# Kernel tuning notes

Measured on AMD Instinct MI355X. Metric: run time of the kernel, lower is better.

Reference implementation:

```python
import jax, jax.numpy as jnp
from jax import lax
import numpy as np


def gen_position(p, pos_decay=1.0):
    # Fixed relative-position bias: (9, p*p), neighbor order di*3+dj
    ar = jnp.arange(p, dtype=jnp.float32)
    right = jnp.broadcast_to(jnp.exp(-ar / (p / pos_decay))[None, :], (p, p))  # decays along width
    down = right.T                                                             # decays along height
    i, j = jnp.meshgrid(ar, ar, indexing='ij')
    br = jnp.exp(-(i + j) / (p / pos_decay))
    ones = jnp.ones((p, p), jnp.float32)
    merge = jnp.stack([
        jnp.rot90(br, 2), down[::-1, :], jnp.rot90(br, 1),
        right[:, ::-1], ones, right,
        jnp.rot90(br, 3), down, br,
    ], axis=0)
    return merge.reshape(9, -1)


def attention_conv(x, w_qkv, b_qkv, head_w, window_size, num_heads):
    b, c, h, w = x.shape
    p = window_size // 3
    pad_h = (p * (1 + h // p) - h) % p
    pad_w = (p * (1 + w // p) - w) % p
    xp = jnp.pad(x, ((0, 0), (0, 0), (p + pad_h, p), (p + pad_w, p)), mode='reflect')
    Hp, Wp = xp.shape[2], xp.shape[3]
    nH, nW = Hp // p - 2, Wp // p - 2  # == number of unfold windows (stride p, size 3p)
    # Non-overlapping p x p tiles; each window = 3x3 grid of adjacent tiles.
    tiles = xp.reshape(b, c, nH + 2, p, nW + 2, p).transpose(0, 2, 4, 1, 3, 5)  # [b,nH+2,nW+2,c,p,p]
    neigh = jnp.stack([tiles[:, di:di + nH, dj:dj + nW]
                       for di in range(3) for dj in range(3)], axis=3)  # [b,nH,nW,9,c,p,p]
    L = c * p * p
    pp = p * p
    xw = neigh.reshape(b * nH * nW, 9, L)
    qkv = xw @ w_qkv.T + b_qkv                                  # [N,9,nh*3*L]
    qkv = qkv.reshape(-1, 9, num_heads, 3, c, pp).transpose(0, 2, 4, 3, 1, 5)  # [N,nh,C,3,9,pp]
    q, k, v = qkv[:, :, :, 0], qkv[:, :, :, 1], qkv[:, :, :, 2]  # each [N,nh,C,9,pp]
    bias = gen_position(p)                                       # [9,pp]
    core_q = q[:, :, :, 4, :]                                    # center patch query [N,nh,C,pp]
    score = jnp.einsum('nhcp,nhckp->nhck', core_q, k * bias) / jnp.sqrt(jnp.float32(L))
    attn = jax.nn.softmax(score, axis=-1)                        # over 9 neighbors
    out = jnp.einsum('nhck,nhckp->nhcp', attn, v).reshape(-1, num_heads, L)
    out = jnp.einsum('h,nhd->nd', head_w[0], out)                # head mixing [N,L]
    out = out.reshape(b, nH, nW, c, p, p).transpose(0, 3, 1, 4, 2, 5).reshape(b, c, nH * p, nW * p)
    return out[:, :, pad_h:, pad_w:]


def setup_inputs() -> dict:
    key = jax.random.key(0)
    ks = jax.random.split(key, 8)
    B, C, H, W = 4, 3, 256, 256
    x = jax.random.uniform(ks[0], (B, C, H, W), dtype=jnp.float32)
    # conv3: window 3, p=1, heads 6, L=3 ; conv6: window 6, p=2, heads 4, L=12 ; conv9: window 9, p=3, heads 2, L=27
    w3_qkv = jax.random.normal(ks[1], (6 * 3 * 3, 3), jnp.float32) * 0.2
    b3_qkv = jnp.zeros((6 * 3 * 3,), jnp.float32)
    hw3 = jnp.full((1, 6), 1.0 / 6.0, jnp.float32)
    w6_qkv = jax.random.normal(ks[2], (4 * 3 * 12, 12), jnp.float32) * 0.1
    b6_qkv = jnp.zeros((4 * 3 * 12,), jnp.float32)
    hw6 = jnp.full((1, 4), 1.0 / 4.0, jnp.float32)
    w9_qkv = jax.random.normal(ks[3], (2 * 3 * 27, 27), jnp.float32) * 0.07
    b9_qkv = jnp.zeros((2 * 3 * 27,), jnp.float32)
    hw9 = jnp.full((1, 2), 1.0 / 2.0, jnp.float32)
    conv0_w = jax.random.normal(ks[4], (3, 9, 5, 5), jnp.float32) * 0.05
    conv0_b = jnp.zeros((3,), jnp.float32)
    return {"x": x, "w3_qkv": w3_qkv, "b3_qkv": b3_qkv, "hw3": hw3,
            "w6_qkv": w6_qkv, "b6_qkv": b6_qkv, "hw6": hw6,
            "w9_qkv": w9_qkv, "b9_qkv": b9_qkv, "hw9": hw9,
            "conv0_w": conv0_w, "conv0_b": conv0_b}


def reference(x, w3_qkv, b3_qkv, hw3, w6_qkv, b6_qkv, hw6,
              w9_qkv, b9_qkv, hw9, conv0_w, conv0_b):
    b, c, h, w = x.shape
    # global prior: softmax over size-1 dim (== ones), then global max pool
    gavg = jnp.mean((1.0 - x).reshape(b, c, -1), axis=-1, keepdims=True)       # [b,c,1]
    x_g = jax.nn.softmax(gavg, axis=-1)[..., None]                             # [b,c,1,1]
    x_g = jnp.max((x * x_g).reshape(b, 1, -1), axis=-1, keepdims=True)[..., None]  # [b,1,1,1]
    x3 = attention_conv(x,  w3_qkv, b3_qkv, hw3, 3, 6)
    x6 = attention_conv(x3, w6_qkv, b6_qkv, hw6, 6, 4)
    x9 = attention_conv(x6, w9_qkv, b9_qkv, hw9, 9, 2)
    cat = jnp.concatenate([x9, x6, x3], axis=1)                                # [b,9,h,w]
    x0 = jax.nn.relu(lax.conv_general_dilated(cat, conv0_w, (1, 1), ((2, 2), (2, 2)),
                                              dimension_numbers=('NCHW', 'OIHW', 'NCHW'))
                     + conv0_b[None, :, None, None])
    return jax.nn.relu(x * x0 + (x_g - x0))
```

## Files before the change

kernel.cpp:

```cpp
#include <hip/hip_runtime.h>
#include <math.h>

__device__ __forceinline__ int refl256(int t) {
    t = t < 0 ? -t : t;
    return t > 255 ? 510 - t : t;
}

__global__ __launch_bounds__(256)
void attn_p1v(const float* __restrict__ x, const float* __restrict__ w,
              const float* __restrict__ bq, const float* __restrict__ hw,
              float* __restrict__ out, float* __restrict__ pmax)
{
    int t = blockIdx.x * 256 + threadIdx.x;
    int xx = t & 255, yp = (t >> 8) & 127, bb = t >> 15;
    int y0 = yp * 2;
    const float* xb = x + bb * 196608;
    int rs[4], cs[3];
#pragma unroll
    for (int dr = 0; dr < 4; ++dr) rs[dr] = refl256(y0 + dr - 1) << 8;
#pragma unroll
    for (int dc = 0; dc < 3; ++dc) cs[dc] = refl256(xx + dc - 1);
    float xw[4][3][3];
#pragma unroll
    for (int dr = 0; dr < 4; ++dr)
#pragma unroll
        for (int dc = 0; dc < 3; ++dc)
#pragma unroll
            for (int c = 0; c < 3; ++c)
                xw[dr][dc][c] = xb[c * 65536 + rs[dr] + cs[dc]];

    {
        float bm = 0.f;
#pragma unroll
        for (int c = 0; c < 3; ++c)
            bm = fmaxf(bm, fmaxf(xw[1][1][c], xw[2][1][c]));
#pragma unroll
        for (int off = 32; off > 0; off >>= 1)
            bm = fmaxf(bm, __shfl_down(bm, off, 64));
        __shared__ float sm[4];
        int lane = threadIdx.x & 63, wid = threadIdx.x >> 6;
        if (lane == 0) sm[wid] = bm;
        __syncthreads();
        if (threadIdx.x == 0)
            pmax[blockIdx.x] = fmaxf(fmaxf(sm[0], sm[1]), fmaxf(sm[2], sm[3]));
    }

    float ov0[3] = {0.f, 0.f, 0.f}, ov1[3] = {0.f, 0.f, 0.f};
    const float scl = 0.57735026919f;
#pragma unroll 1
    for (int h = 0; h < 6; ++h) {
        float hwh = hw[h];
#pragma unroll
        for (int cc = 0; cc < 3; ++cc) {
            int oq = 9 * h + cc, ok = oq + 3, oV = oq + 6;
            float wq0 = w[oq * 3], wq1 = w[oq * 3 + 1], wq2 = w[oq * 3 + 2];
            float wk0 = w[ok * 3], wk1 = w[ok * 3 + 1], wk2 = w[ok * 3 + 2];
            float wv0 = w[oV * 3], wv1 = w[oV * 3 + 1], wv2 = w[oV * 3 + 2];
            float bk = bq[ok], bv = bq[oV];
            float kp[12], vp[12];
#pragma unroll
            for (int pos = 0; pos < 12; ++pos) {
                const float* xv = xw[pos / 3][pos % 3];
                kp[pos] = fmaf(xv[0], wk0, fmaf(xv[1], wk1, fmaf(xv[2], wk2, bk)));
                vp[pos] = fmaf(xv[0], wv0, fmaf(xv[1], wv1, fmaf(xv[2], wv2, bv)));
            }
            float q0 = fmaf(xw[1][1][0], wq0, fmaf(xw[1][1][1], wq1, fmaf(xw[1][1][2], wq2, bq[oq]))) * scl;
            float q1 = fmaf(xw[2][1][0], wq0, fmaf(xw[2][1][1], wq1, fmaf(xw[2][1][2], wq2, bq[oq]))) * scl;
            float se0 = 0.f, ac0 = 0.f, se1 = 0.f, ac1 = 0.f;
#pragma unroll
            for (int j = 0; j < 9; ++j) {
                float e0 = __expf(q0 * kp[j]);
                se0 += e0; ac0 = fmaf(e0, vp[j], ac0);
                float e1 = __expf(q1 * kp[3 + j]);
                se1 += e1; ac1 = fmaf(e1, vp[3 + j], ac1);
            }
            ov0[cc] = fmaf(hwh, ac0 / se0, ov0[cc]);
            ov1[cc] = fmaf(hwh, ac1 / se1, ov1[cc]);
        }
    }
    int pix = (y0 << 8) + xx;
    float* ob = out + bb * 196608;
#pragma unroll
    for (int cc = 0; cc < 3; ++cc) {
        ob[cc * 65536 + pix] = ov0[cc];
        ob[cc * 65536 + pix + 256] = ov1[cc];
    }
}

template<int P, int NH, int NWIN, int OFS, int GSU, int NCH>
__global__ __launch_bounds__(64 * NCH)
void proj3_pk(const float* __restrict__ x, const float* __restrict__ w,
              const float* __restrict__ bq, float* __restrict__ kv)
{
    constexpr int PP = P * P, L = 3 * PP, NO = NH * 9 * PP, NG = NO / GSU;
    constexpr int CPG = NG / NCH;
    constexpr int NT = NWIN + 2, T4 = 4 * NT * NT;
    int t = blockIdx.x * 64 + threadIdx.x;
    if (t >= T4) return;
    const int chunk = __builtin_amdgcn_readfirstlane((int)threadIdx.y);
    int bb = t / (NT * NT), rr = t - bb * NT * NT;
    int ty = rr / NT, tx = rr - ty * NT;
    const float* xb = x + bb * 196608;
    float xw[L];
#pragma unroll
    for (int i = 0; i < P; ++i) {
        int pr = refl256(ty * P + i - OFS) << 8;
#pragma unroll
        for (int j = 0; j < P; ++j) {
            int pc = refl256(tx * P + j - OFS);
#pragma unroll
            for (int c = 0; c < 3; ++c)
                xw[c * PP + i * P + j] = xb[c * 65536 + pr + pc];
        }
    }
    float4* dst = (float4*)kv + t + (size_t)chunk * CPG * T4;
#pragma unroll 1
    for (int g = 0; g < CPG; ++g) {
        int go = (chunk * CPG + g) * GSU;
        float acc[GSU];
#pragma unroll
        for (int e = 0; e < GSU; ++e) acc[e] = bq[go + e];
#pragma unroll
        for (int l = 0; l < L; ++l) {
            float xv = xw[l];
#pragma unroll
            for (int e = 0; e < GSU; ++e)
                acc[e] = fmaf(xv, w[(go + e) * L + l], acc[e]);
        }
        float4 o4;
        o4.x = acc[0];
        o4.y = acc[1];
        o4.z = acc[2];
        o4.w = (GSU == 4) ? acc[GSU - 1] : 0.f;
        dst[(size_t)g * T4] = o4;
    }
}

template<int P, int NH, int NWIN, int OFS, int GSU>
__global__ __launch_bounds__(256)
void attn2_pk(const float* __restrict__ kv, const float* __restrict__ hw,
              float* __restrict__ out)
{
    constexpr int PP = P * P, NT = NWIN + 2, T4 = 4 * NT * NT, PAD = OFS - P;
    constexpr int NGP = (PP + GSU - 1) / GSU;
    constexpr float SCL = (P == 2) ? 0.28867513459481287f : 0.19245008972987526f;
    constexpr float DD  = (P == 2) ? 0.6065306597126334f : 0.7165313105737893f;
    float dpw[2 * P - 1];
    dpw[0] = 1.f;
#pragma unroll
    for (int k = 1; k < 2 * P - 1; ++k) dpw[k] = dpw[k - 1] * DD;

    int tid = threadIdx.x;
    int wlin = blockIdx.x * 256 + tid;
    if (wlin >= 4 * NWIN * NWIN) return;
    int c = blockIdx.y;
    int bb = wlin / (NWIN * NWIN); int rr = wlin - bb * NWIN * NWIN;
    int yy = rr / NWIN, xx = rr - yy * NWIN;
    int tbase = bb * NT * NT + yy * NT + xx;
    int tn[9];
#pragma unroll
    for (int di = 0; di < 3; ++di)
#pragma unroll
        for (int dj = 0; dj < 3; ++dj) tn[di * 3 + dj] = tbase + di * NT + dj;
    const float4* kv4 = (const float4*)kv;
    float oa[PP];
#pragma unroll
    for (int e = 0; e < PP; ++e) oa[e] = 0.f;
#pragma unroll 1
    for (int h = 0; h < NH; ++h) {
        int oq = ((h * 3 + 0) * 3 + c) * PP;
        int ok = ((h * 3 + 1) * 3 + c) * PP;
        int ov = ((h * 3 + 2) * 3 + c) * PP;
        int gq = oq / GSU, gk = ok / GSU, gv = ov / GSU;
        float q[PP];
#pragma unroll
        for (int u = 0; u < NGP; ++u) {
            float4 t4 = kv4[(size_t)(gq + u) * T4 + tn[4]];
            float g4[4] = {t4.x, t4.y, t4.z, t4.w};
#pragma unroll
            for (int e = 0; e < GSU; ++e) q[u * GSU + e] = g4[e];
        }
        float sc[9];
#pragma unroll
        for (int j = 0; j < 9; ++j) {
            int di = j / 3, dj = j - di * 3;
            float s = 0.f;
#pragma unroll
            for (int u = 0; u < NGP; ++u) {
                float4 t4 = kv4[(size_t)(gk + u) * T4 + tn[j]];
                float g4[4] = {t4.x, t4.y, t4.z, t4.w};
#pragma unroll
                for (int e = 0; e < GSU; ++e) {
                    int Pp = u * GSU + e;
                    int i = Pp / P, jj = Pp - i * P;
                    int er = (di == 0) ? (P - 1 - i) : (di == 2 ? i : 0);
                    int ec = (dj == 0) ? (P - 1 - jj) : (dj == 2 ? jj : 0);
                    s = fmaf(q[Pp] * g4[e], dpw[er + ec], s);
                }
            }
            sc[j] = s * SCL;
        }
        float se = 0.f;
#pragma unroll
        for (int j = 0; j < 9; ++j) { sc[j] = __expf(sc[j]); se += sc[j]; }
        float tmp[PP];
#pragma unroll
        for (int e = 0; e < PP; ++e) tmp[e] = 0.f;
#pragma unroll
        for (int j = 0; j < 9; ++j) {
#pragma unroll
            for (int u = 0; u < NGP; ++u) {
                float4 t4 = kv4[(size_t)(gv + u) * T4 + tn[j]];
                float g4[4] = {t4.x, t4.y, t4.z, t4.w};
#pragma unroll
                for (int e = 0; e < GSU; ++e)
                    tmp[u * GSU + e] = fmaf(sc[j], g4[e], tmp[u * GSU + e]);
            }
        }
        float f = hw[h] / se;
#pragma unroll
        for (int e = 0; e < PP; ++e) oa[e] = fmaf(f, tmp[e], oa[e]);
    }
    float* ob = out + (bb * 3 + c) * 65536;
#pragma unroll
    for (int i = 0; i < P; ++i) {
        int r = yy * P + i - PAD;
        if (PAD && r < 0) continue;
#pragma unroll
        for (int jj = 0; jj < P; ++jj) {
            int col = xx * P + jj - PAD;
            if (PAD && col < 0) continue;
            ob[(r << 8) + col] = oa[i * P + jj];
        }
    }
}

__global__ __launch_bounds__(256)
void conv_finalv2(const float* __restrict__ x, const float* __restrict__ x9,
                  const float* __restrict__ x6, const float* __restrict__ x3,
                  const float* __restrict__ cw, const float* __restrict__ cb,
                  const float* __restrict__ pmax, float* __restrict__ out)
{
    int tid = threadIdx.x;
    int bb = blockIdx.x >> 7;
    __shared__ float red[128];
    __shared__ float s_g;
    if (tid < 128) red[tid] = pmax[bb * 128 + tid];
    __syncthreads();
    if (tid < 64) {
        float v = fmaxf(red[tid], red[tid + 64]);
#pragma unroll
        for (int off = 32; off > 0; off >>= 1)
            v = fmaxf(v, __shfl_down(v, off, 64));
        if (tid == 0) s_g = v;
    }
    __syncthreads();

    int gid = blockIdx.x * 256 + tid;
    int xp = (gid & 127) << 1, r = (gid >> 7) & 255;
    float a[3][2];
#pragma unroll
    for (int oc = 0; oc < 3; ++oc) {
        float b = cb[oc];
        a[oc][0] = b; a[oc][1] = b;
    }
#pragma unroll 1
    for (int s = 0; s < 3; ++s) {
        const float* bp = (s == 0 ? x9 : (s == 1 ? x6 : x3)) + bb * 196608;
#pragma unroll 1
        for (int c2 = 0; c2 < 3; ++c2) {
            const float* pl = bp + c2 * 65536;
            const float* wp = cw + (s * 3 + c2) * 25;
#pragma unroll
            for (int ky = 0; ky < 5; ++ky) {
                int rr = r + ky - 2;
                if ((unsigned)rr >= 256u) continue;
                const float* row = pl + (rr << 8);
                float2 va = (xp >= 2) ? *(const float2*)(row + xp - 2)
                                      : make_float2(0.f, 0.f);
                float2 vb = *(const float2*)(row + xp);
                float2 vc = (xp + 2 < 256) ? *(const float2*)(row + xp + 2)
                                           : make_float2(0.f, 0.f);
                float cv[6] = {va.x, va.y, vb.x, vb.y, vc.x, vc.y};
#pragma unroll
                for (int kx = 0; kx < 5; ++kx) {
                    float w0 = wp[ky * 5 + kx];
                    float w1 = wp[225 + ky * 5 + kx];
                    float w2 = wp[450 + ky * 5 + kx];
                    float v0 = cv[kx], v1 = cv[kx + 1];
                    a[0][0] = fmaf(v0, w0, a[0][0]); a[0][1] = fmaf(v1, w0, a[0][1]);
                    a[1][0] = fmaf(v0, w1, a[1][0]); a[1][1] = fmaf(v1, w1, a[1][1]);
                    a[2][0] = fmaf(v0, w2, a[2][0]); a[2][1] = fmaf(v1, w2, a[2][1]);
                }
            }
        }
    }
    float g = s_g;
    int pix = (r << 8) + xp;
    const float* xb = x + bb * 196608;
    float* ob = out + bb * 196608;
#pragma unroll
    for (int oc = 0; oc < 3; ++oc) {
        float2 xv = *(const float2*)(xb + oc * 65536 + pix);
        float2 o2;
        float x0;
        x0 = fmaxf(a[oc][0], 0.f); o2.x = fmaxf(xv.x * x0 + g - x0, 0.f);
        x0 = fmaxf(a[oc][1], 0.f); o2.y = fmaxf(xv.y * x0 + g - x0, 0.f);
        *(float2*)(ob + oc * 65536 + pix) = o2;
    }
}

extern "C" void kernel_launch(void* const* d_in, const int* in_sizes, int n_in,
                              void* d_out, int out_size, void* d_ws, size_t ws_size,
                              hipStream_t stream)
{
    const float* x   = (const float*)d_in[0];
    const float* w3  = (const float*)d_in[1];
    const float* b3  = (const float*)d_in[2];
    const float* hw3 = (const float*)d_in[3];
    const float* w6  = (const float*)d_in[4];
    const float* b6  = (const float*)d_in[5];
    const float* hw6 = (const float*)d_in[6];
    const float* w9  = (const float*)d_in[7];
    const float* b9  = (const float*)d_in[8];
    const float* hw9 = (const float*)d_in[9];
    const float* cw  = (const float*)d_in[10];
    const float* cb  = (const float*)d_in[11];

    float* ws   = (float*)d_ws;
    float* x3b  = ws;
    float* x6b  = ws + 786432;
    float* x9b  = ws + 1572864;
    float* pmax = ws + 2359296;
    float* kvb  = ws + 2359808;
    float* out  = (float*)d_out;

    attn_p1v<<<512, 256, 0, stream>>>(x, w3, b3, hw3, x3b, pmax);

    proj3_pk<2, 4, 128, 2, 4, 6><<<1057, dim3(64, 6), 0, stream>>>(x3b, w6, b6, kvb);
    attn2_pk<2, 4, 128, 2, 4><<<dim3(256, 3), 256, 0, stream>>>(kvb, hw6, x6b);
    proj3_pk<3, 2, 86, 5, 3, 9><<<484, dim3(64, 9), 0, stream>>>(x6b, w9, b9, kvb);
    attn2_pk<3, 2, 86, 5, 3><<<dim3(116, 3), 256, 0, stream>>>(kvb, hw9, x9b);

    conv_finalv2<<<512, 256, 0, stream>>>(x, x9b, x6b, x3b, cw, cb, pmax, out);
}
```

Measured before the change: 171.5 us.

## Split heads and conv sources across thread groups with shared-memory reduction

Splits the per-pixel work in the first attention kernel, both packed attention kernels and the final conv across 2-3 thread groups (by head group or conv source). Partial sums are combined through shared memory, so each launch has twice as many blocks and each thread has a shorter serial loop. The aim is more parallelism and better latency hiding, since these grids were small relative to the GPU. The cost is an extra __syncthreads, shared-memory traffic, and idle threads during the final write. The pmax buffer doubles in size, so the kv workspace offset moves.

Measured after the change: 157.5 us. -8.2%, faster.

```diff
diff --git a/kernel.cpp b/kernel.cpp
--- a/kernel.cpp
+++ b/kernel.cpp
@@ -7,12 +7,14 @@
 }
 
 __global__ __launch_bounds__(256)
-void attn_p1v(const float* __restrict__ x, const float* __restrict__ w,
-              const float* __restrict__ bq, const float* __restrict__ hw,
-              float* __restrict__ out, float* __restrict__ pmax)
-{
-    int t = blockIdx.x * 256 + threadIdx.x;
-    int xx = t & 255, yp = (t >> 8) & 127, bb = t >> 15;
+void attn_p1v2(const float* __restrict__ x, const float* __restrict__ w,
+               const float* __restrict__ bq, const float* __restrict__ hw,
+               float* __restrict__ out, float* __restrict__ pmax)
+{
+    const int slot = threadIdx.x;
+    const int hg = __builtin_amdgcn_readfirstlane((int)threadIdx.y);
+    int t2 = blockIdx.x * 128 + slot;
+    int xx = t2 & 255, yp = (t2 >> 8) & 127, bb = t2 >> 15;
     int y0 = yp * 2;
     const float* xb = x + bb * 196608;
     int rs[4], cs[3];
@@ -38,17 +40,18 @@
         for (int off = 32; off > 0; off >>= 1)
             bm = fmaxf(bm, __shfl_down(bm, off, 64));
         __shared__ float sm[4];
-        int lane = threadIdx.x & 63, wid = threadIdx.x >> 6;
-        if (lane == 0) sm[wid] = bm;
+        int flat = threadIdx.y * 128 + slot;
+        if ((flat & 63) == 0) sm[flat >> 6] = bm;
         __syncthreads();
-        if (threadIdx.x == 0)
+        if (flat == 0)
             pmax[blockIdx.x] = fmaxf(fmaxf(sm[0], sm[1]), fmaxf(sm[2], sm[3]));
     }
 
     float ov0[3] = {0.f, 0.f, 0.f}, ov1[3] = {0.f, 0.f, 0.f};
     const float scl = 0.57735026919f;
 #pragma unroll 1
-    for (int h = 0; h < 6; ++h) {
+    for (int hi = 0; hi < 3; ++hi) {
+        int h = hg * 3 + hi;
         float hwh = hw[h];
 #pragma unroll
         for (int cc = 0; cc < 3; ++cc) {
@@ -78,12 +81,23 @@
             ov1[cc] = fmaf(hwh, ac1 / se1, ov1[cc]);
         }
     }
-    int pix = (y0 << 8) + xx;
-    float* ob = out + bb * 196608;
-#pragma unroll
-    for (int cc = 0; cc < 3; ++cc) {
-        ob[cc * 65536 + pix] = ov0[cc];
-        ob[cc * 65536 + pix + 256] = ov1[cc];
+    __shared__ float s_part[128][6];
+    if (hg == 1) {
+#pragma unroll
+        for (int cc = 0; cc < 3; ++cc) {
+            s_part[slot][cc] = ov0[cc];
+            s_part[slot][3 + cc] = ov1[cc];
+        }
+    }
+    __syncthreads();
+    if (hg == 0) {
+        int pix = (y0 << 8) + xx;
+        float* ob = out + bb * 196608;
+#pragma unroll
+        for (int cc = 0; cc < 3; ++cc) {
+            ob[cc * 65536 + pix] = ov0[cc] + s_part[slot][cc];
+            ob[cc * 65536 + pix + 256] = ov1[cc] + s_part[slot][3 + cc];
+        }
     }
 }
 
@@ -136,9 +150,9 @@
     }
 }
 
-template<int P, int NH, int NWIN, int OFS, int GSU>
+template<int P, int NH, int NWIN, int OFS, int GSU, int HPT>
 __global__ __launch_bounds__(256)
-void attn2_pk(const float* __restrict__ kv, const float* __restrict__ hw,
+void attn3_pk(const float* __restrict__ kv, const float* __restrict__ hw,
               float* __restrict__ out)
 {
     constexpr int PP = P * P, NT = NWIN + 2, T4 = 4 * NT * NT, PAD = OFS - P;
@@ -150,11 +164,13 @@
 #pragma unroll
     for (int k = 1; k < 2 * P - 1; ++k) dpw[k] = dpw[k - 1] * DD;
 
-    int tid = threadIdx.x;
-    int wlin = blockIdx.x * 256 + tid;
-    if (wlin >= 4 * NWIN * NWIN) return;
+    const int slot = threadIdx.x;
+    const int hg = __builtin_amdgcn_readfirstlane((int)threadIdx.y);
+    int wlin = blockIdx.x * 128 + slot;
+    const bool active = wlin < 4 * NWIN * NWIN;
+    int wsafe = active ? wlin : 0;
     int c = blockIdx.y;
-    int bb = wlin / (NWIN * NWIN); int rr = wlin - bb * NWIN * NWIN;
+    int bb = wsafe / (NWIN * NWIN); int rr = wsafe - bb * (NWIN * NWIN);
     int yy = rr / NWIN, xx = rr - yy * NWIN;
     int tbase = bb * NT * NT + yy * NT + xx;
     int tn[9];
@@ -167,7 +183,8 @@
 #pragma unroll
     for (int e = 0; e < PP; ++e) oa[e] = 0.f;
 #pragma unroll 1
-    for (int h = 0; h < NH; ++h) {
+    for (int hi = 0; hi < HPT; ++hi) {
+        int h = hg * HPT + hi;
         int oq = ((h * 3 + 0) * 3 + c) * PP;
         int ok = ((h * 3 + 1) * 3 + c) * PP;
         int ov = ((h * 3 + 2) * 3 + c) * PP;
@@ -221,92 +238,108 @@
 #pragma unroll
         for (int e = 0; e < PP; ++e) oa[e] = fmaf(f, tmp[e], oa[e]);
     }
-    float* ob = out + (bb * 3 + c) * 65536;
-#pragma unroll
-    for (int i = 0; i < P; ++i) {
-        int r = yy * P + i - PAD;
-        if (PAD && r < 0) continue;
-#pragma unroll
-        for (int jj = 0; jj < P; ++jj) {
-            int col = xx * P + jj - PAD;
-            if (PAD && col < 0) continue;
-            ob[(r << 8) + col] = oa[i * P + jj];
-        }
-    }
-}
-
-__global__ __launch_bounds__(256)
-void conv_finalv2(const float* __restrict__ x, const float* __restrict__ x9,
+    __shared__ float s_part[128][PP];
+    if (hg == 1) {
+#pragma unroll
+        for (int e = 0; e < PP; ++e) s_part[slot][e] = oa[e];
+    }
+    __syncthreads();
+    if (hg == 0 && active) {
+        float* ob = out + (bb * 3 + c) * 65536;
+#pragma unroll
+        for (int i = 0; i < P; ++i) {
+            int r = yy * P + i - PAD;
+            if (PAD && r < 0) continue;
+#pragma unroll
+            for (int jj = 0; jj < P; ++jj) {
+                int col = xx * P + jj - PAD;
+                if (PAD && col < 0) continue;
+                int e = i * P + jj;
+                ob[(r << 8) + col] = oa[e] + s_part[slot][e];
+            }
+        }
+    }
+}
+
+__global__ __launch_bounds__(384)
+void conv_finalv3(const float* __restrict__ x, const float* __restrict__ x9,
                   const float* __restrict__ x6, const float* __restrict__ x3,
                   const float* __restrict__ cw, const float* __restrict__ cb,
                   const float* __restrict__ pmax, float* __restrict__ out)
 {
-    int tid = threadIdx.x;
-    int bb = blockIdx.x >> 7;
-    __shared__ float red[128];
+    const int slot = threadIdx.x;
+    const int src = __builtin_amdgcn_readfirstlane((int)threadIdx.y);
+    int bb = blockIdx.x >> 8;
     __shared__ float s_g;
-    if (tid < 128) red[tid] = pmax[bb * 128 + tid];
+    {
+        int flat = threadIdx.y * 128 + slot;
+        if (flat < 64) {
+            const float* pm = pmax + bb * 256 + flat * 4;
+            float v = fmaxf(fmaxf(pm[0], pm[1]), fmaxf(pm[2], pm[3]));
+#pragma unroll
+            for (int off = 32; off > 0; off >>= 1)
+                v = fmaxf(v, __shfl_down(v, off, 64));
+            if (flat == 0) s_g = v;
+        }
+    }
+    int pair = (blockIdx.x & 255) * 128 + slot;
+    int xp = (pair & 127) << 1, r = pair >> 7;
+    float a[3][2];
+#pragma unroll
+    for (int oc = 0; oc < 3; ++oc) { a[oc][0] = 0.f; a[oc][1] = 0.f; }
+    const float* bp = (src == 0 ? x9 : (src == 1 ? x6 : x3)) + bb * 196608;
+#pragma unroll 1
+    for (int c2 = 0; c2 < 3; ++c2) {
+        const float* pl = bp + c2 * 65536;
+        const float* wp = cw + (src * 3 + c2) * 25;
+#pragma unroll
+        for (int ky = 0; ky < 5; ++ky) {
+            int rr = r + ky - 2;
+            if ((unsigned)rr >= 256u) continue;
+            const float* row = pl + (rr << 8);
+            float2 va = (xp >= 2) ? *(const float2*)(row + xp - 2)
+                                  : make_float2(0.f, 0.f);
+            float2 vb = *(const float2*)(row + xp);
+            float2 vc = (xp + 2 < 256) ? *(const float2*)(row + xp + 2)
+                                       : make_float2(0.f, 0.f);
+            float cv[6] = {va.x, va.y, vb.x, vb.y, vc.x, vc.y};
+#pragma unroll
+            for (int kx = 0; kx < 5; ++kx) {
+                float w0 = wp[ky * 5 + kx];
+                float w1 = wp[225 + ky * 5 + kx];
+                float w2 = wp[450 + ky * 5 + kx];
+                float v0 = cv[kx], v1 = cv[kx + 1];
+                a[0][0] = fmaf(v0, w0, a[0][0]); a[0][1] = fmaf(v1, w0, a[0][1]);
+                a[1][0] = fmaf(v0, w1, a[1][0]); a[1][1] = fmaf(v1, w1, a[1][1]);
+                a[2][0] = fmaf(v0, w2, a[2][0]); a[2][1] = fmaf(v1, w2, a[2][1]);
+            }
+        }
+    }
+    __shared__ float s_part[2][128][6];
+    if (src > 0) {
+#pragma unroll
+        for (int oc = 0; oc < 3; ++oc) {
+            s_part[src - 1][slot][oc * 2]     = a[oc][0];
+            s_part[src - 1][slot][oc * 2 + 1] = a[oc][1];
+        }
+    }
     __syncthreads();
-    if (tid < 64) {
-        float v = fmaxf(red[tid], red[tid + 64]);
-#pragma unroll
-        for (int off = 32; off > 0; off >>= 1)
-            v = fmaxf(v, __shfl_down(v, off, 64));
-        if (tid == 0) s_g = v;
-    }
-    __syncthreads();
-
-    int gid = blockIdx.x * 256 + tid;
-    int xp = (gid & 127) << 1, r = (gid >> 7) & 255;
-    float a[3][2];
-#pragma unroll
-    for (int oc = 0; oc < 3; ++oc) {
-        float b = cb[oc];
-        a[oc][0] = b; a[oc][1] = b;
-    }
-#pragma unroll 1
-    for (int s = 0; s < 3; ++s) {
-        const float* bp = (s == 0 ? x9 : (s == 1 ? x6 : x3)) + bb * 196608;
-#pragma unroll 1
-        for (int c2 = 0; c2 < 3; ++c2) {
-            const float* pl = bp + c2 * 65536;
-            const float* wp = cw + (s * 3 + c2) * 25;
-#pragma unroll
-            for (int ky = 0; ky < 5; ++ky) {
-                int rr = r + ky - 2;
-                if ((unsigned)rr >= 256u) continue;
-                const float* row = pl + (rr << 8);
-                float2 va = (xp >= 2) ? *(const float2*)(row + xp - 2)
-                                      : make_float2(0.f, 0.f);
-                float2 vb = *(const float2*)(row + xp);
-                float2 vc = (xp + 2 < 256) ? *(const float2*)(row + xp + 2)
-                                           : make_float2(0.f, 0.f);
-                float cv[6] = {va.x, va.y, vb.x, vb.y, vc.x, vc.y};
-#pragma unroll
-                for (int kx = 0; kx < 5; ++kx) {
-                    float w0 = wp[ky * 5 + kx];
-                    float w1 = wp[225 + ky * 5 + kx];
-                    float w2 = wp[450 + ky * 5 + kx];
-                    float v0 = cv[kx], v1 = cv[kx + 1];
-                    a[0][0] = fmaf(v0, w0, a[0][0]); a[0][1] = fmaf(v1, w0, a[0][1]);
-                    a[1][0] = fmaf(v0, w1, a[1][0]); a[1][1] = fmaf(v1, w1, a[1][1]);
-                    a[2][0] = fmaf(v0, w2, a[2][0]); a[2][1] = fmaf(v1, w2, a[2][1]);
-                }
-            }
-        }
-    }
-    float g = s_g;
-    int pix = (r << 8) + xp;
-    const float* xb = x + bb * 196608;
-    float* ob = out + bb * 196608;
-#pragma unroll
-    for (int oc = 0; oc < 3; ++oc) {
-        float2 xv = *(const float2*)(xb + oc * 65536 + pix);
-        float2 o2;
-        float x0;
-        x0 = fmaxf(a[oc][0], 0.f); o2.x = fmaxf(xv.x * x0 + g - x0, 0.f);
-        x0 = fmaxf(a[oc][1], 0.f); o2.y = fmaxf(xv.y * x0 + g - x0, 0.f);
-        *(float2*)(ob + oc * 65536 + pix) = o2;
+    if (src == 0) {
+        float g = s_g;
+        int pix = (r << 8) + xp;
+        const float* xb = x + bb * 196608;
+        float* ob = out + bb * 196608;
+#pragma unroll
+        for (int oc = 0; oc < 3; ++oc) {
+            float a0 = a[oc][0] + s_part[0][slot][oc * 2] + s_part[1][slot][oc * 2] + cb[oc];
+            float a1 = a[oc][1] + s_part[0][slot][oc * 2 + 1] + s_part[1][slot][oc * 2 + 1] + cb[oc];
+            float2 xv = *(const float2*)(xb + oc * 65536 + pix);
+            float2 o2;
+            float x0;
+            x0 = fmaxf(a0, 0.f); o2.x = fmaxf(xv.x * x0 + g - x0, 0.f);
+            x0 = fmaxf(a1, 0.f); o2.y = fmaxf(xv.y * x0 + g - x0, 0.f);
+            *(float2*)(ob + oc * 65536 + pix) = o2;
+        }
     }
 }
 
@@ -332,15 +365,15 @@
     float* x6b  = ws + 786432;
     float* x9b  = ws + 1572864;
     float* pmax = ws + 2359296;
-    float* kvb  = ws + 2359808;
+    float* kvb  = ws + 2360320;
     float* out  = (float*)d_out;
 
-    attn_p1v<<<512, 256, 0, stream>>>(x, w3, b3, hw3, x3b, pmax);
+    attn_p1v2<<<1024, dim3(128, 2), 0, stream>>>(x, w3, b3, hw3, x3b, pmax);
 
     proj3_pk<2, 4, 128, 2, 4, 6><<<1057, dim3(64, 6), 0, stream>>>(x3b, w6, b6, kvb);
-    attn2_pk<2, 4, 128, 2, 4><<<dim3(256, 3), 256, 0, stream>>>(kvb, hw6, x6b);
+    attn3_pk<2, 4, 128, 2, 4, 2><<<dim3(512, 3), dim3(128, 2), 0, stream>>>(kvb, hw6, x6b);
     proj3_pk<3, 2, 86, 5, 3, 9><<<484, dim3(64, 9), 0, stream>>>(x6b, w9, b9, kvb);
-    attn2_pk<3, 2, 86, 5, 3><<<dim3(116, 3), 256, 0, stream>>>(kvb, hw9, x9b);
-
-    conv_finalv2<<<512, 256, 0, stream>>>(x, x9b, x6b, x3b, cw, cb, pmax, out);
-}
+    attn3_pk<3, 2, 86, 5, 3, 1><<<dim3(232, 3), dim3(128, 2), 0, stream>>>(kvb, hw9, x9b);
+
+    conv_finalv3<<<1024, dim3(128, 3), 0, stream>>>(x, x9b, x6b, x3b, cw, cb, pmax, out);
+}
```
